# Kernel optimization log

Measured on AMD Instinct MI355X. Metric: run time of the kernel, lower is better.

The kernel has to match this reference:

```python
import jax, jax.numpy as jnp
import numpy as np
import math

B, S, H = 2, 4096, 768
NH, HD = 12, 64  # num heads, head dim


def setup_inputs() -> dict:
    key = jax.random.key(0)
    ks = jax.random.split(key, 4)
    scale = 1.0 / math.sqrt(H)
    return {
        "hidden_states": jax.random.normal(ks[0], (B, S, H), jnp.float32),
        "attention_mask": jnp.zeros((B, 1, 1, S), jnp.float32),
        "Wq": jax.random.normal(ks[1], (H, H), jnp.float32) * scale,
        "bq": jnp.zeros((H,), jnp.float32),
        "Wk": jax.random.normal(ks[2], (H, H), jnp.float32) * scale,
        "bk": jnp.zeros((H,), jnp.float32),
        "Wv": jax.random.normal(ks[3], (H, H), jnp.float32) * scale,
        "bv": jnp.zeros((H,), jnp.float32),
    }


def reference(hidden_states, attention_mask, Wq, bq, Wk, bk, Wv, bv):
    # Linear projections (torch nn.Linear: x @ W.T + b)
    q = hidden_states @ Wq.T + bq  # [B,S,H]
    k = hidden_states @ Wk.T + bk
    v = hidden_states @ Wv.T + bv
    # split heads -> [B, NH, S, HD]
    def split(x):
        return x.reshape(B, S, NH, HD).transpose(0, 2, 1, 3)
    qh, kh, vh = split(q), split(k), split(v)
    scores = jnp.einsum('bhqd,bhkd->bhqk', qh, kh) / math.sqrt(HD)
    scores = scores + attention_mask  # additive mask, broadcast
    probs = jax.nn.softmax(scores, axis=-1)
    # dropout prob = 0.0 (inference) -> identity
    ctx = jnp.einsum('bhqk,bhkd->bhqd', probs, vh)
    ctx = ctx.transpose(0, 2, 1, 3).reshape(B, S, H)
    return ctx
```

## Files before the change

### kernel.cpp

```cpp
#include <hip/hip_runtime.h>
#include <hip/hip_bf16.h>

typedef float f32x4 __attribute__((ext_vector_type(4)));
typedef float f32x16 __attribute__((ext_vector_type(16)));
typedef short short8 __attribute__((ext_vector_type(8)));

#define LOG2E 1.44269504088896340736f

__device__ __forceinline__ ushort f2bf(float f){
  unsigned u = __builtin_bit_cast(unsigned, f);
  u = (u + 0x7fffu + ((u >> 16) & 1u)) >> 16;
  return (ushort)u;
}

__device__ __forceinline__ float exp2_hw(float x){
  float r; asm("v_exp_f32 %0, %1" : "=v"(r) : "v"(x)); return r;
}

__device__ __forceinline__ uint pack_bf16_rh(float lo, float hi){
  uint ul = __builtin_bit_cast(uint, lo) + 0x8000u;
  uint uh = __builtin_bit_cast(uint, hi) + 0x8000u;
  return __builtin_amdgcn_perm(uh, ul, 0x07060302u);
}

__device__ __forceinline__ float fmax3(float a, float b, float c){
  return fmaxf(fmaxf(a, b), c);
}

__global__ void cvt_kernel(const float* __restrict__ src, ushort* __restrict__ dst, int n4){
  int i = blockIdx.x * 256 + threadIdx.x;
  if (i < n4){
    float4 v = ((const float4*)src)[i];
    ushort4 o; o.x = f2bf(v.x); o.y = f2bf(v.y); o.z = f2bf(v.z); o.w = f2bf(v.w);
    ((ushort4*)dst)[i] = o;
  }
}

__global__ void scale_kernel(const float* __restrict__ src, float* __restrict__ dst,
                             float sc, int n){
  int i = blockIdx.x * 256 + threadIdx.x;
  if (i < n) dst[i] = src[i] * sc;
}

__global__ __launch_bounds__(256) void qkv_gemm(const ushort* __restrict__ Xb,
                                                const ushort* __restrict__ Wb,
                                                const float* __restrict__ bias,
                                                ushort* __restrict__ Out,
                                                float scale){
  __shared__ ushort Xs[128*64];
  __shared__ ushort Ws[128*64];
  const int m0 = blockIdx.x * 128, n0 = blockIdx.y * 128;
  const int tid = threadIdx.x, w = tid >> 6, lane = tid & 63;
  const int r = lane & 15, g = lane >> 4;
  const int wr = (w >> 1) * 64, wc = (w & 1) * 64;
  f32x4 acc[4][4] = {};
  for (int k0 = 0; k0 < 768; k0 += 64){
    #pragma unroll
    for (int p = 0; p < 4; p++){
      int c = tid + 256*p; int row = c >> 3, cir = c & 7;
      uint4 vx = *(const uint4*)(Xb + (size_t)(m0+row)*768 + k0 + cir*8);
      *(uint4*)((char*)Xs + row*128 + ((cir*16) ^ ((row&7)<<4))) = vx;
      uint4 vw = *(const uint4*)(Wb + (size_t)(n0+row)*768 + k0 + cir*8);
      *(uint4*)((char*)Ws + row*128 + ((cir*16) ^ ((row&7)<<4))) = vw;
    }
    __syncthreads();
    #pragma unroll
    for (int ks = 0; ks < 2; ks++){
      short8 af[4], bf[4];
      int bo = ks*64 + g*16;
      #pragma unroll
      for (int i = 0; i < 4; i++){
        int rowa = wr + i*16 + r;
        af[i] = *(const short8*)((char*)Xs + rowa*128 + (bo ^ ((rowa&7)<<4)));
        int rowb = wc + i*16 + r;
        bf[i] = *(const short8*)((char*)Ws + rowb*128 + (bo ^ ((rowb&7)<<4)));
      }
      #pragma unroll
      for (int i = 0; i < 4; i++)
        #pragma unroll
        for (int j = 0; j < 4; j++)
          acc[i][j] = __builtin_amdgcn_mfma_f32_16x16x32_bf16(af[i], bf[j], acc[i][j], 0,0,0);
    }
    __syncthreads();
  }
  #pragma unroll
  for (int i = 0; i < 4; i++){
    #pragma unroll
    for (int j = 0; j < 4; j++){
      int col = n0 + wc + j*16 + r;
      float bv = bias[col];
      int rowb = m0 + wr + i*16 + g*4;
      #pragma unroll
      for (int q = 0; q < 4; q++)
        Out[(size_t)(rowb+q)*768 + col] = f2bf((acc[i][j][q] + bv) * scale);
    }
  }
}

__global__ __launch_bounds__(256) void qkv_gemm_vt(const ushort* __restrict__ Xb,
                                                   const ushort* __restrict__ Wb,
                                                   const float* __restrict__ bias,
                                                   ushort* __restrict__ VtOut){
  __shared__ ushort Xs[128*64];
  __shared__ ushort Ws[128*64];
  const int m0 = blockIdx.x * 128, n0 = blockIdx.y * 128;
  const int tid = threadIdx.x, w = tid >> 6, lane = tid & 63;
  const int r = lane & 15, g = lane >> 4;
  const int wr = (w >> 1) * 64, wc = (w & 1) * 64;
  f32x4 acc[4][4] = {};
  for (int k0 = 0; k0 < 768; k0 += 64){
    #pragma unroll
    for (int p = 0; p < 4; p++){
      int c = tid + 256*p; int row = c >> 3, cir = c & 7;
      uint4 vx = *(const uint4*)(Xb + (size_t)(m0+row)*768 + k0 + cir*8);
      *(uint4*)((char*)Xs + row*128 + ((cir*16) ^ ((row&7)<<4))) = vx;
      uint4 vw = *(const uint4*)(Wb + (size_t)(n0+row)*768 + k0 + cir*8);
      *(uint4*)((char*)Ws + row*128 + ((cir*16) ^ ((row&7)<<4))) = vw;
    }
    __syncthreads();
    #pragma unroll
    for (int ks = 0; ks < 2; ks++){
      short8 af[4], bf[4];
      int bo = ks*64 + g*16;
      #pragma unroll
      for (int i = 0; i < 4; i++){
        int rowa = wr + i*16 + r;
        af[i] = *(const short8*)((char*)Xs + rowa*128 + (bo ^ ((rowa&7)<<4)));
        int rowb = wc + i*16 + r;
        bf[i] = *(const short8*)((char*)Ws + rowb*128 + (bo ^ ((rowb&7)<<4)));
      }
      #pragma unroll
      for (int i = 0; i < 4; i++)
        #pragma unroll
        for (int j = 0; j < 4; j++)
          acc[i][j] = __builtin_amdgcn_mfma_f32_16x16x32_bf16(af[i], bf[j], acc[i][j], 0,0,0);
    }
    __syncthreads();
  }
  #pragma unroll
  for (int i = 0; i < 4; i++){
    #pragma unroll
    for (int j = 0; j < 4; j++){
      int col = n0 + wc + j*16 + r;
      float bv = bias[col];
      int rowb = m0 + wr + i*16 + g*4;
      ushort4 o;
      o.x = f2bf(acc[i][j][0] + bv);
      o.y = f2bf(acc[i][j][1] + bv);
      o.z = f2bf(acc[i][j][2] + bv);
      o.w = f2bf(acc[i][j][3] + bv);
      size_t vrow = (size_t)((rowb >> 12) * 768 + col);
      *(ushort4*)(VtOut + vrow * 4096 + (rowb & 4095)) = o;
    }
  }
}

__global__ __launch_bounds__(256, 3) void flash_attn(const ushort* __restrict__ Qb,
                                                     const ushort* __restrict__ Kb,
                                                     const ushort* __restrict__ Vt,
                                                     const float* __restrict__ maskL,
                                                     float* __restrict__ out){
  __shared__ ushort Ks[64*64];
  __shared__ ushort Vts[64*64];
  const int tid = threadIdx.x, w = tid >> 6, lane = tid & 63;
  const int q = lane & 31, hi = lane >> 5;
  const int swq = (q & 7) << 4;
  const int h = blockIdx.y, b = blockIdx.z;
  const int q0 = blockIdx.x * 128 + w * 32;

  short8 bq[4];
  {
    const ushort* qp = Qb + (size_t)(b*4096 + q0 + q)*768 + h*64 + hi*8;
    #pragma unroll
    for (int kd = 0; kd < 4; kd++) bq[kd] = *(const short8*)(qp + 16*kd);
  }
  const ushort* Kbase = Kb + (size_t)(b*4096)*768 + h*64;
  const ushort* Vbase = Vt + (size_t)(b*768 + h*64)*4096;

  const int row0 = tid >> 3, cir = tid & 7;
  const int row1 = row0 + 32;

  uint4 kreg0, kreg1, vreg0, vreg1;
  kreg0 = *(const uint4*)(Kbase + (size_t)row0*768 + cir*8);
  kreg1 = *(const uint4*)(Kbase + (size_t)row1*768 + cir*8);
  vreg0 = *(const uint4*)(Vbase + (size_t)row0*4096 + cir*8);
  vreg1 = *(const uint4*)(Vbase + (size_t)row1*4096 + cir*8);

  f32x16 ctx[2] = {};
  float mrun = -1e30f, lrun = 0.f;

  for (int t = 0; t < 64; t++){
    const int kv0 = t * 64;
    *(uint4*)((char*)Ks  + row0*128 + ((cir*16) ^ ((row0&7)<<4))) = kreg0;
    *(uint4*)((char*)Ks  + row1*128 + ((cir*16) ^ ((row1&7)<<4))) = kreg1;
    *(uint4*)((char*)Vts + row0*128 + ((cir*16) ^ ((row0&7)<<4))) = vreg0;
    *(uint4*)((char*)Vts + row1*128 + ((cir*16) ^ ((row1&7)<<4))) = vreg1;
    __syncthreads();
    if (t < 63){
      const int kn = kv0 + 64;
      kreg0 = *(const uint4*)(Kbase + (size_t)(kn+row0)*768 + cir*8);
      kreg1 = *(const uint4*)(Kbase + (size_t)(kn+row1)*768 + cir*8);
      vreg0 = *(const uint4*)(Vbase + (size_t)row0*4096 + kn + cir*8);
      vreg1 = *(const uint4*)(Vbase + (size_t)row1*4096 + kn + cir*8);
    }
    f32x16 sc[2];
    #pragma unroll
    for (int s = 0; s < 2; s++){
      f32x16 z = {};
      #pragma unroll
      for (int kd = 0; kd < 4; kd++){
        int row = s*32 + q;
        short8 ak = *(const short8*)((char*)Ks + row*128 + ((32*kd + 16*hi) ^ swq));
        z = __builtin_amdgcn_mfma_f32_32x32x16_bf16(ak, bq[kd], z, 0,0,0);
      }
      sc[s] = z;
    }
    #pragma unroll
    for (int s = 0; s < 2; s++)
      #pragma unroll
      for (int eq = 0; eq < 4; eq++){
        float4 mv = *(const float4*)(maskL + b*4096 + kv0 + s*32 + eq*8 + hi*4);
        sc[s][4*eq+0] += mv.x; sc[s][4*eq+1] += mv.y;
        sc[s][4*eq+2] += mv.z; sc[s][4*eq+3] += mv.w;
      }
    float ma = fmax3(sc[0][0], sc[0][1], sc[0][2]);
    float mb = fmax3(sc[0][3], sc[0][4], sc[0][5]);
    ma = fmax3(ma, sc[0][6], sc[0][7]);
    mb = fmax3(mb, sc[0][8], sc[0][9]);
    ma = fmax3(ma, sc[0][10], sc[0][11]);
    mb = fmax3(mb, sc[0][12], sc[0][13]);
    ma = fmax3(ma, sc[0][14], sc[0][15]);
    #pragma unroll
    for (int e = 0; e < 15; e += 3) mb = fmax3(mb, sc[1][e], sc[1][e+1]);
    ma = fmax3(ma, sc[1][2], sc[1][5]);
    ma = fmax3(ma, sc[1][8], sc[1][11]);
    ma = fmax3(ma, sc[1][14], sc[1][15]);
    float mt = fmaxf(ma, mb);
    mt = fmaxf(mt, __shfl_xor(mt, 32, 64));
    if (!__all(mt <= mrun + 11.5415603f)){
      float mnew = fmaxf(mrun, mt);
      float alpha = exp2_hw(mrun - mnew);
      mrun = mnew;
      lrun *= alpha;
      #pragma unroll
      for (int s = 0; s < 2; s++)
        #pragma unroll
        for (int e = 0; e < 16; e++) ctx[s][e] *= alpha;
    }
    float rs = 0.f;
    #pragma unroll
    for (int s = 0; s < 2; s++)
      #pragma unroll
      for (int e = 0; e < 16; e++){
        float pv = exp2_hw(sc[s][e] - mrun); sc[s][e] = pv; rs += pv;
      }
    rs += __shfl_xor(rs, 32, 64);
    lrun += rs;
    short8 bp[4];
    #pragma unroll
    for (int s = 0; s < 2; s++){
      uint pw[8];
      #pragma unroll
      for (int u = 0; u < 8; u++)
        pw[u] = pack_bf16_rh(sc[s][2*u], sc[s][2*u+1]);
      #pragma unroll
      for (int u2 = 0; u2 < 2; u2++){
        uint x0 = pw[4*u2+0], x1 = pw[4*u2+1], x2 = pw[4*u2+2], x3 = pw[4*u2+3];
        asm("v_permlane32_swap_b32 %0, %1" : "+v"(x0), "+v"(x2));
        asm("v_permlane32_swap_b32 %0, %1" : "+v"(x1), "+v"(x3));
        union { uint u[4]; short8 v; } bb;
        bb.u[0] = x0; bb.u[1] = x1; bb.u[2] = x2; bb.u[3] = x3;
        bp[2*s + u2] = bb.v;
      }
    }
    #pragma unroll
    for (int sd = 0; sd < 2; sd++){
      int row = sd*32 + q;
      #pragma unroll
      for (int kk = 0; kk < 4; kk++){
        short8 av = *(const short8*)((char*)Vts + row*128 + ((32*kk + 16*hi) ^ swq));
        ctx[sd] = __builtin_amdgcn_mfma_f32_32x32x16_bf16(av, bp[kk], ctx[sd], 0,0,0);
      }
    }
    __syncthreads();
  }
  float inv = 1.0f / lrun;
  size_t orow = (size_t)(b*4096 + q0 + q) * 768 + h*64;
  #pragma unroll
  for (int sd = 0; sd < 2; sd++)
    #pragma unroll
    for (int eq = 0; eq < 4; eq++){
      float4 o;
      o.x = ctx[sd][4*eq+0] * inv; o.y = ctx[sd][4*eq+1] * inv;
      o.z = ctx[sd][4*eq+2] * inv; o.w = ctx[sd][4*eq+3] * inv;
      *(float4*)(out + orow + sd*32 + eq*8 + hi*4) = o;
    }
}

extern "C" void kernel_launch(void* const* d_in, const int* in_sizes, int n_in,
                              void* d_out, int out_size, void* d_ws, size_t ws_size,
                              hipStream_t stream){
  const float* hidden = (const float*)d_in[0];
  const float* mask   = (const float*)d_in[1];
  const float* Wq     = (const float*)d_in[2];
  const float* bq     = (const float*)d_in[3];
  const float* Wk     = (const float*)d_in[4];
  const float* bk     = (const float*)d_in[5];
  const float* Wv     = (const float*)d_in[6];
  const float* bv     = (const float*)d_in[7];
  char* ws = (char*)d_ws;
  ushort* Xb    = (ushort*)(ws);
  ushort* Wqb   = (ushort*)(ws + 12582912);
  ushort* Wkb   = (ushort*)(ws + 13762560);
  ushort* Wvb   = (ushort*)(ws + 14942208);
  ushort* Qb    = (ushort*)(ws + 16121856);
  ushort* Kb    = (ushort*)(ws + 28704768);
  ushort* Vtb   = (ushort*)(ws + 41287680);
  float*  maskL = (float*)(ws + 53870592);

  cvt_kernel<<<6144, 256, 0, stream>>>(hidden, Xb, 1572864);
  cvt_kernel<<<576, 256, 0, stream>>>(Wq, Wqb, 147456);
  cvt_kernel<<<576, 256, 0, stream>>>(Wk, Wkb, 147456);
  cvt_kernel<<<576, 256, 0, stream>>>(Wv, Wvb, 147456);
  scale_kernel<<<32, 256, 0, stream>>>(mask, maskL, LOG2E, 8192);

  dim3 gg(64, 6);
  qkv_gemm<<<gg, 256, 0, stream>>>(Xb, Wqb, bq, Qb, 0.125f * LOG2E);
  qkv_gemm<<<gg, 256, 0, stream>>>(Xb, Wkb, bk, Kb, 1.0f);
  qkv_gemm_vt<<<gg, 256, 0, stream>>>(Xb, Wvb, bv, Vtb);

  dim3 ga(32, 12, 2);
  flash_attn<<<ga, 256, 0, stream>>>(Qb, Kb, Vtb, maskL, (float*)d_out);
}
```

Before: 240.6 us.

## Double-buffer K/V in flash attention and fuse X conversion into Q GEMM

The flash attention kernel now keeps two LDS buffers for K and V tiles. The next tile is written to LDS while the current one is being computed on, which removes one barrier per iteration. The QK and PV MFMA sections are wrapped in s_setprio to favour matrix issue. The separate fp32-to-bf16 conversion of hidden_states is folded into the Q projection GEMM, which reads fp32 directly and writes the bf16 copy from the blockIdx.y==0 blocks. This saves a kernel launch and one pass over X, at the cost of doubled LDS use (possible occupancy loss) and fp32 reads in the Q GEMM.

Result: slower. 245.6 us (+2.1%).

```diff
diff --git a/kernel.cpp b/kernel.cpp
--- a/kernel.cpp
+++ b/kernel.cpp
@@ -21,6 +21,10 @@
   uint ul = __builtin_bit_cast(uint, lo) + 0x8000u;
   uint uh = __builtin_bit_cast(uint, hi) + 0x8000u;
   return __builtin_amdgcn_perm(uh, ul, 0x07060302u);
+}
+
+__device__ __forceinline__ uint pack_bf16_rne(float lo, float hi){
+  return ((uint)f2bf(lo)) | (((uint)f2bf(hi)) << 16);
 }
 
 __device__ __forceinline__ float fmax3(float a, float b, float c){
@@ -40,6 +44,72 @@
                              float sc, int n){
   int i = blockIdx.x * 256 + threadIdx.x;
   if (i < n) dst[i] = src[i] * sc;
+}
+
+__global__ __launch_bounds__(256) void qkv_gemm_qx(const float* __restrict__ Xf,
+                                                   const ushort* __restrict__ Wb,
+                                                   const float* __restrict__ bias,
+                                                   ushort* __restrict__ Out,
+                                                   ushort* __restrict__ XbOut,
+                                                   float scale){
+  __shared__ ushort Xs[128*64];
+  __shared__ ushort Ws[128*64];
+  const int m0 = blockIdx.x * 128, n0 = blockIdx.y * 128;
+  const int tid = threadIdx.x, w = tid >> 6, lane = tid & 63;
+  const int r = lane & 15, g = lane >> 4;
+  const int wr = (w >> 1) * 64, wc = (w & 1) * 64;
+  const bool writeX = (blockIdx.y == 0);
+  f32x4 acc[4][4] = {};
+  for (int k0 = 0; k0 < 768; k0 += 64){
+    #pragma unroll
+    for (int p = 0; p < 4; p++){
+      int c = tid + 256*p; int row = c >> 3, cir = c & 7;
+      const float* xp = Xf + (size_t)(m0+row)*768 + k0 + cir*8;
+      float4 x0 = *(const float4*)xp;
+      float4 x1 = *(const float4*)(xp + 4);
+      uint4 vx;
+      vx.x = pack_bf16_rne(x0.x, x0.y);
+      vx.y = pack_bf16_rne(x0.z, x0.w);
+      vx.z = pack_bf16_rne(x1.x, x1.y);
+      vx.w = pack_bf16_rne(x1.z, x1.w);
+      *(uint4*)((char*)Xs + row*128 + ((cir*16) ^ ((row&7)<<4))) = vx;
+      if (writeX)
+        *(uint4*)((ushort*)XbOut + (size_t)(m0+row)*768 + k0 + cir*8) = vx;
+      uint4 vw = *(const uint4*)(Wb + (size_t)(n0+row)*768 + k0 + cir*8);
+      *(uint4*)((char*)Ws + row*128 + ((cir*16) ^ ((row&7)<<4))) = vw;
+    }
+    __syncthreads();
+    #pragma unroll
+    for (int ks = 0; ks < 2; ks++){
+      short8 af[4], bf[4];
+      int bo = ks*64 + g*16;
+      #pragma unroll
+      for (int i = 0; i < 4; i++){
+        int rowa = wr + i*16 + r;
+        af[i] = *(const short8*)((char*)Xs + rowa*128 + (bo ^ ((rowa&7)<<4)));
+        int rowb = wc + i*16 + r;
+        bf[i] = *(const short8*)((char*)Ws + rowb*128 + (bo ^ ((rowb&7)<<4)));
+      }
+      #pragma unroll
+      for (int i = 0; i < 4; i++)
+        #pragma unroll
+        for (int j = 0; j < 4; j++)
+          acc[i][j] = __builtin_amdgcn_mfma_f32_16x16x32_bf16(af[i], bf[j], acc[i][j], 0,0,0);
+    }
+    __syncthreads();
+  }
+  #pragma unroll
+  for (int i = 0; i < 4; i++){
+    #pragma unroll
+    for (int j = 0; j < 4; j++){
+      int col = n0 + wc + j*16 + r;
+      float bv = bias[col];
+      int rowb = m0 + wr + i*16 + g*4;
+      #pragma unroll
+      for (int q = 0; q < 4; q++)
+        Out[(size_t)(rowb+q)*768 + col] = f2bf((acc[i][j][q] + bv) * scale);
+    }
+  }
 }
 
 __global__ __launch_bounds__(256) void qkv_gemm(const ushort* __restrict__ Xb,
@@ -160,8 +230,8 @@
                                                      const ushort* __restrict__ Vt,
                                                      const float* __restrict__ maskL,
                                                      float* __restrict__ out){
-  __shared__ ushort Ks[64*64];
-  __shared__ ushort Vts[64*64];
+  __shared__ ushort Ks[2][64*64];
+  __shared__ ushort Vts[2][64*64];
   const int tid = threadIdx.x, w = tid >> 6, lane = tid & 63;
   const int q = lane & 31, hi = lane >> 5;
   const int swq = (q & 7) << 4;
@@ -179,42 +249,61 @@
 
   const int row0 = tid >> 3, cir = tid & 7;
   const int row1 = row0 + 32;
+  const int wb0 = row0*128 + ((cir*16) ^ ((row0&7)<<4));
+  const int wb1 = row1*128 + ((cir*16) ^ ((row1&7)<<4));
 
   uint4 kreg0, kreg1, vreg0, vreg1;
   kreg0 = *(const uint4*)(Kbase + (size_t)row0*768 + cir*8);
   kreg1 = *(const uint4*)(Kbase + (size_t)row1*768 + cir*8);
   vreg0 = *(const uint4*)(Vbase + (size_t)row0*4096 + cir*8);
   vreg1 = *(const uint4*)(Vbase + (size_t)row1*4096 + cir*8);
+  *(uint4*)((char*)Ks[0]  + wb0) = kreg0;
+  *(uint4*)((char*)Ks[0]  + wb1) = kreg1;
+  *(uint4*)((char*)Vts[0] + wb0) = vreg0;
+  *(uint4*)((char*)Vts[0] + wb1) = vreg1;
+  kreg0 = *(const uint4*)(Kbase + (size_t)(64+row0)*768 + cir*8);
+  kreg1 = *(const uint4*)(Kbase + (size_t)(64+row1)*768 + cir*8);
+  vreg0 = *(const uint4*)(Vbase + (size_t)row0*4096 + 64 + cir*8);
+  vreg1 = *(const uint4*)(Vbase + (size_t)row1*4096 + 64 + cir*8);
+  __syncthreads();
 
   f32x16 ctx[2] = {};
   float mrun = -1e30f, lrun = 0.f;
 
   for (int t = 0; t < 64; t++){
-    const int kv0 = t * 64;
-    *(uint4*)((char*)Ks  + row0*128 + ((cir*16) ^ ((row0&7)<<4))) = kreg0;
-    *(uint4*)((char*)Ks  + row1*128 + ((cir*16) ^ ((row1&7)<<4))) = kreg1;
-    *(uint4*)((char*)Vts + row0*128 + ((cir*16) ^ ((row0&7)<<4))) = vreg0;
-    *(uint4*)((char*)Vts + row1*128 + ((cir*16) ^ ((row1&7)<<4))) = vreg1;
-    __syncthreads();
+    const int cur = t & 1;
+    const char* Kc = (const char*)Ks[cur];
+    const char* Vc = (const char*)Vts[cur];
+    f32x16 sc[2];
+    __builtin_amdgcn_s_setprio(1);
+    #pragma unroll
+    for (int s = 0; s < 2; s++){
+      f32x16 z = {};
+      #pragma unroll
+      for (int kd = 0; kd < 4; kd++){
+        int row = s*32 + q;
+        short8 ak = *(const short8*)(Kc + row*128 + ((32*kd + 16*hi) ^ swq));
+        z = __builtin_amdgcn_mfma_f32_32x32x16_bf16(ak, bq[kd], z, 0,0,0);
+      }
+      sc[s] = z;
+    }
+    __builtin_amdgcn_s_setprio(0);
     if (t < 63){
-      const int kn = kv0 + 64;
+      char* Kn = (char*)Ks[cur^1];
+      char* Vn = (char*)Vts[cur^1];
+      *(uint4*)(Kn + wb0) = kreg0;
+      *(uint4*)(Kn + wb1) = kreg1;
+      *(uint4*)(Vn + wb0) = vreg0;
+      *(uint4*)(Vn + wb1) = vreg1;
+    }
+    if (t < 62){
+      const int kn = (t+2) * 64;
       kreg0 = *(const uint4*)(Kbase + (size_t)(kn+row0)*768 + cir*8);
       kreg1 = *(const uint4*)(Kbase + (size_t)(kn+row1)*768 + cir*8);
       vreg0 = *(const uint4*)(Vbase + (size_t)row0*4096 + kn + cir*8);
       vreg1 = *(const uint4*)(Vbase + (size_t)row1*4096 + kn + cir*8);
     }
-    f32x16 sc[2];
-    #pragma unroll
-    for (int s = 0; s < 2; s++){
-      f32x16 z = {};
-      #pragma unroll
-      for (int kd = 0; kd < 4; kd++){
-        int row = s*32 + q;
-        short8 ak = *(const short8*)((char*)Ks + row*128 + ((32*kd + 16*hi) ^ swq));
-        z = __builtin_amdgcn_mfma_f32_32x32x16_bf16(ak, bq[kd], z, 0,0,0);
-      }
-      sc[s] = z;
-    }
+    const int kv0 = t * 64;
     #pragma unroll
     for (int s = 0; s < 2; s++)
       #pragma unroll
@@ -273,15 +362,17 @@
         bp[2*s + u2] = bb.v;
       }
     }
+    __builtin_amdgcn_s_setprio(1);
     #pragma unroll
     for (int sd = 0; sd < 2; sd++){
       int row = sd*32 + q;
       #pragma unroll
       for (int kk = 0; kk < 4; kk++){
-        short8 av = *(const short8*)((char*)Vts + row*128 + ((32*kk + 16*hi) ^ swq));
+        short8 av = *(const short8*)(Vc + row*128 + ((32*kk + 16*hi) ^ swq));
         ctx[sd] = __builtin_amdgcn_mfma_f32_32x32x16_bf16(av, bp[kk], ctx[sd], 0,0,0);
       }
     }
+    __builtin_amdgcn_s_setprio(0);
     __syncthreads();
   }
   float inv = 1.0f / lrun;
@@ -318,14 +409,13 @@
   ushort* Vtb   = (ushort*)(ws + 41287680);
   float*  maskL = (float*)(ws + 53870592);
 
-  cvt_kernel<<<6144, 256, 0, stream>>>(hidden, Xb, 1572864);
   cvt_kernel<<<576, 256, 0, stream>>>(Wq, Wqb, 147456);
   cvt_kernel<<<576, 256, 0, stream>>>(Wk, Wkb, 147456);
   cvt_kernel<<<576, 256, 0, stream>>>(Wv, Wvb, 147456);
   scale_kernel<<<32, 256, 0, stream>>>(mask, maskL, LOG2E, 8192);
 
   dim3 gg(64, 6);
-  qkv_gemm<<<gg, 256, 0, stream>>>(Xb, Wqb, bq, Qb, 0.125f * LOG2E);
+  qkv_gemm_qx<<<gg, 256, 0, stream>>>(hidden, Wqb, bq, Qb, Xb, 0.125f * LOG2E);
   qkv_gemm<<<gg, 256, 0, stream>>>(Xb, Wkb, bk, Kb, 1.0f);
   qkv_gemm_vt<<<gg, 256, 0, stream>>>(Xb, Wvb, bv, Vtb);
 
```
